# Performance work log

Measured on AMD Instinct MI355X. Metric: run time of the kernel, lower is better.

The kernel has to match this reference:

```python
import jax, jax.numpy as jnp
import numpy as np

N_HEADS, D_MODEL, D_HEAD = 16, 1024, 64
EPSILON = -100000.0  # module uses -1e5, not -inf
INIT_STD = 0.02


def setup_inputs() -> dict:
    key = jax.random.key(0)
    ks = jax.random.split(key, 5)
    B, S = 4, 2048
    x = jax.random.normal(ks[0], (B, S, D_MODEL), dtype=jnp.float32)
    W_Q = INIT_STD * jax.random.normal(ks[1], (N_HEADS, D_MODEL, D_HEAD), dtype=jnp.float32)
    W_K = INIT_STD * jax.random.normal(ks[2], (N_HEADS, D_MODEL, D_HEAD), dtype=jnp.float32)
    W_V = INIT_STD * jax.random.normal(ks[3], (N_HEADS, D_MODEL, D_HEAD), dtype=jnp.float32)
    W_O = INIT_STD * jax.random.normal(ks[4], (N_HEADS, D_HEAD, D_MODEL), dtype=jnp.float32)
    b_Q = jnp.zeros((N_HEADS, D_HEAD), jnp.float32)
    b_K = jnp.zeros((N_HEADS, D_HEAD), jnp.float32)
    b_V = jnp.zeros((N_HEADS, D_HEAD), jnp.float32)
    b_O = jnp.zeros((D_MODEL,), jnp.float32)
    return {"normalized_resid_pre": x, "W_Q": W_Q, "b_Q": b_Q, "W_K": W_K,
            "b_K": b_K, "W_V": W_V, "b_V": b_V, "W_O": W_O, "b_O": b_O}


def reference(normalized_resid_pre, W_Q, b_Q, W_K, b_K, W_V, b_V, W_O, b_O):
    x = normalized_resid_pre  # [b, s, e]
    q = jnp.einsum('bse,neh->bsnh', x, W_Q) + b_Q
    k = jnp.einsum('bse,neh->bsnh', x, W_K) + b_K
    v = jnp.einsum('bse,neh->bsnh', x, W_V) + b_V
    scores = jnp.einsum('bqnh,bknh->bnqk', q, k) / jnp.sqrt(jnp.float32(D_HEAD))
    sq, sk = scores.shape[-2], scores.shape[-1]
    causal = jnp.triu(jnp.ones((sq, sk), bool), k=1)  # True above diagonal
    scores = jnp.where(causal, jnp.float32(EPSILON), scores)
    probs = jax.nn.softmax(scores, axis=-1)
    z = jnp.einsum('bnqk,bknh->bqnh', probs, v)
    # sum over heads of per-head output projection + bias
    attn_out = jnp.einsum('bqnh,nhe->bqe', z, W_O) + b_O
    return attn_out
```

## Files before the change

kernel.cpp:

```cpp
#include <hip/hip_runtime.h>


typedef __attribute__((ext_vector_type(8))) short short8;
typedef __attribute__((ext_vector_type(4))) float floatx4;

#define SCL 0.1803368801111244f

__device__ __forceinline__ unsigned short f2bf(float f) {
  unsigned int x = __float_as_uint(f);
  x += 0x7fffu + ((x >> 16) & 1u);
  return (unsigned short)(x >> 16);
}

__device__ __forceinline__ void gload_lds16(const unsigned short* g, unsigned short* lds) {
  __builtin_amdgcn_global_load_lds(
      (const __attribute__((address_space(1))) void*)g,
      (__attribute__((address_space(3))) void*)lds, 16, 0, 0);
}

__global__ __launch_bounds__(256) void cvt_x_kernel(const float* __restrict__ X,
                                                    unsigned short* __restrict__ Xb) {
  int idx = ((blockIdx.x << 8) + threadIdx.x) << 2;
  float4 f = *(const float4*)(X + idx);
  unsigned short u[4] = { f2bf(f.x), f2bf(f.y), f2bf(f.z), f2bf(f.w) };
  *(uint2*)(Xb + idx) = *(uint2*)u;
}

__global__ __launch_bounds__(256) void transpose_wqkv3(
    const float* __restrict__ Wq, const float* __restrict__ Wk,
    const float* __restrict__ Wv, unsigned short* __restrict__ Bt) {
  __shared__ unsigned short T[64 * 72];
  const int t = threadIdx.x;
  const int e0 = blockIdx.x << 6, nn = blockIdx.y, proj = blockIdx.z;
  const float* W = (proj == 0) ? Wq : (proj == 1) ? Wk : Wv;
  const float* src = W + ((size_t)nn << 16) + ((size_t)e0 << 6);
#pragma unroll
  for (int rnd = 0; rnd < 4; ++rnd) {
    int off = (rnd << 10) + (t << 2);
    float4 f = *(const float4*)(src + off);
    int r = off >> 6, h = off & 63;
    T[r * 72 + h]     = f2bf(f.x);
    T[r * 72 + h + 1] = f2bf(f.y);
    T[r * 72 + h + 2] = f2bf(f.z);
    T[r * 72 + h + 3] = f2bf(f.w);
  }
  __syncthreads();
  const int h = t >> 2, ck = t & 3;
  size_t orow = ((size_t)((proj << 10) + (nn << 6) + h) << 10) + e0 + (ck << 4);
#pragma unroll
  for (int g = 0; g < 2; ++g) {
    unsigned short v[8];
#pragma unroll
    for (int j = 0; j < 8; ++j) v[j] = T[((ck << 4) + (g << 3) + j) * 72 + h];
    *(int4*)(Bt + orow + (g << 3)) = *(int4*)v;
  }
}

__global__ __launch_bounds__(256) void transpose_wo(const float* __restrict__ W,
                                                    unsigned short* __restrict__ Wt) {
  __shared__ unsigned short T[64 * 72];
  const int t = threadIdx.x;
  const int e0 = blockIdx.x << 6, k0 = blockIdx.y << 6;
#pragma unroll
  for (int rnd = 0; rnd < 4; ++rnd) {
    int r = (rnd << 4) + (t >> 4);
    int c = (t & 15) << 2;
    float4 f = *(const float4*)(W + ((size_t)(k0 + r) << 10) + e0 + c);
    T[r * 72 + c]     = f2bf(f.x);
    T[r * 72 + c + 1] = f2bf(f.y);
    T[r * 72 + c + 2] = f2bf(f.z);
    T[r * 72 + c + 3] = f2bf(f.w);
  }
  __syncthreads();
  const int i = t >> 2, ck = t & 3;
  size_t orow = ((size_t)(e0 + i) << 10) + k0 + (ck << 4);
#pragma unroll
  for (int g = 0; g < 2; ++g) {
    unsigned short v[8];
#pragma unroll
    for (int j = 0; j < 8; ++j) v[j] = T[((ck << 4) + (g << 3) + j) * 72 + i];
    *(int4*)(Wt + orow + (g << 3)) = *(int4*)v;
  }
}

template <int MODE>
__global__ __launch_bounds__(256) void gemm128_kernel(
    const unsigned short* __restrict__ A,
    const unsigned short* __restrict__ Bt,
    const float* __restrict__ b0, const float* __restrict__ b1,
    const float* __restrict__ b2,
    unsigned short* __restrict__ Oq, unsigned short* __restrict__ Ok,
    unsigned short* __restrict__ Ov, float* __restrict__ Of)
{
  const int K = 1024;
  __shared__ __align__(16) unsigned short As[4096];
  __shared__ __align__(16) unsigned short Bs[4096];
  const int tid = threadIdx.x;
  const int l   = tid & 63, w = tid >> 6;
  const int l15 = l & 15,  lg = l >> 4;
  const int mo  = (w >> 1) << 6, no = (w & 1) << 6;
  const int m0  = blockIdx.y << 7, n0 = blockIdx.x << 7;
  const int lrow = l >> 2;
  const int lcol = (l & 3) << 3;

  floatx4 acc[4][4];
#pragma unroll
  for (int i = 0; i < 4; ++i)
#pragma unroll
    for (int j = 0; j < 4; ++j) acc[i][j] = (floatx4){0.f, 0.f, 0.f, 0.f};

  for (int k0 = 0; k0 < K; k0 += 32) {
    __syncthreads();
#pragma unroll
    for (int j = 0; j < 2; ++j) {
      int seg = (w << 1) + j;
      int row = (seg << 4) + lrow;
      gload_lds16(A  + (size_t)(m0 + row) * K + k0 + lcol, &As[seg << 9]);
      gload_lds16(Bt + (size_t)(n0 + row) * K + k0 + lcol, &Bs[seg << 9]);
    }
    __syncthreads();
    short8 af[4], bf[4];
#pragma unroll
    for (int mc = 0; mc < 4; ++mc)
      af[mc] = *(const short8*)&As[((mo + (mc << 4) + l15) << 5) + (lg << 3)];
#pragma unroll
    for (int nc = 0; nc < 4; ++nc)
      bf[nc] = *(const short8*)&Bs[((no + (nc << 4) + l15) << 5) + (lg << 3)];
#pragma unroll
    for (int mc = 0; mc < 4; ++mc)
#pragma unroll
      for (int nc = 0; nc < 4; ++nc)
        acc[mc][nc] = __builtin_amdgcn_mfma_f32_16x16x32_bf16(af[mc], bf[nc], acc[mc][nc], 0, 0, 0);
  }

#pragma unroll
  for (int nc = 0; nc < 4; ++nc) {
    int c = n0 + no + (nc << 4) + l15;
    if (MODE == 1) {
      float bv = b0[c];
#pragma unroll
      for (int mc = 0; mc < 4; ++mc)
#pragma unroll
        for (int r = 0; r < 4; ++r) {
          int m = m0 + mo + (mc << 4) + (lg << 2) + r;
          Of[((size_t)m << 10) + c] = acc[mc][nc][r] + bv;
        }
    } else {
      int proj = c >> 10, cc = c & 1023;
      int hn = cc >> 6, h = cc & 63;
      const float* bp = (proj == 0) ? b0 : (proj == 1) ? b1 : b2;
      float bv = bp[cc];
      float sc = (proj == 0) ? SCL : 1.0f;
      if (proj < 2) {
        unsigned short* O = (proj == 0) ? Oq : Ok;
#pragma unroll
        for (int mc = 0; mc < 4; ++mc)
#pragma unroll
          for (int r = 0; r < 4; ++r) {
            int m = m0 + mo + (mc << 4) + (lg << 2) + r;
            int bb = m >> 11, ss = m & 2047;
            O[((((size_t)(bb << 4) + hn) << 11) + ss) * 64 + h] = f2bf((acc[mc][nc][r] + bv) * sc);
          }
      } else {
#pragma unroll
        for (int mc = 0; mc < 4; ++mc) {
          int m = m0 + mo + (mc << 4) + (lg << 2);
          int bb = m >> 11, ss = m & 2047;
          unsigned short p0 = f2bf(acc[mc][nc][0] + bv);
          unsigned short p1 = f2bf(acc[mc][nc][1] + bv);
          unsigned short p2 = f2bf(acc[mc][nc][2] + bv);
          unsigned short p3 = f2bf(acc[mc][nc][3] + bv);
          uint2 pk;
          pk.x = (unsigned int)p0 | ((unsigned int)p1 << 16);
          pk.y = (unsigned int)p2 | ((unsigned int)p3 << 16);
          *(uint2*)&Ov[((((size_t)(bb << 4) + hn) << 6) + h) * 2048 + ss] = pk;
        }
      }
    }
  }
}

__global__ __launch_bounds__(256, 2) void flash3_kernel(
    const unsigned short* __restrict__ Q,
    const unsigned short* __restrict__ K,
    const unsigned short* __restrict__ Vt,
    unsigned short* __restrict__ Z)
{
  __shared__ __align__(16) unsigned short Ks[4096];
  __shared__ __align__(16) unsigned short Vs[4096];
  __shared__ __align__(16) unsigned short Ps[4 * 2304];

  const int tid = threadIdx.x;
  const int l   = tid & 63, w = tid >> 6;
  const int l15 = l & 15,  lg = l >> 4;
  const int x    = blockIdx.x;
  const int head = ((x & 7) << 3) + ((x >> 6) & 7);
  const int pairidx = (x >> 3) & 7;
  const int n = head & 15, b = head >> 4;
  const size_t hoff = (size_t)head << 17;
  const unsigned short* Qh = Q + hoff;
  const unsigned short* Kh = K + hoff;
  const unsigned short* Vh = Vt + hoff;
  unsigned short* Psw = Ps + w * 2304;

  const int srow8 = l >> 3;
  const int sblk8 = ((l & 7) ^ srow8) << 3;
  const int swz   = l15 & 7;
  const int bo0   = (lg ^ swz) << 3;
  const int bo1   = ((4 + lg) ^ swz) << 3;

  short8 onef;
#pragma unroll
  for (int i = 0; i < 8; ++i) onef[i] = (short)0x3F80;

  for (int half = 0; half < 2; ++half) {
    const int qt  = half ? (15 - pairidx) : pairidx;
    const int q0w = (qt << 7) + (w << 5);

    short8 qf[2][2];
#pragma unroll
    for (int qc = 0; qc < 2; ++qc)
#pragma unroll
      for (int dh = 0; dh < 2; ++dh)
        qf[qc][dh] = *(const short8*)(Qh + (size_t)(q0w + (qc << 4) + l15) * 64 + (dh << 5) + (lg << 3));

    floatx4 acc_o[2][4], acc_l[2];
#pragma unroll
    for (int qc = 0; qc < 2; ++qc) {
      acc_l[qc] = (floatx4){0.f, 0.f, 0.f, 0.f};
#pragma unroll
      for (int dc = 0; dc < 4; ++dc) acc_o[qc][dc] = (floatx4){0.f, 0.f, 0.f, 0.f};
    }

    const int nkt = (qt << 1) + 2;
    for (int kt = 0; kt < nkt; ++kt) {
      const int k0 = kt << 6;
      __syncthreads();
#pragma unroll
      for (int j = 0; j < 2; ++j) {
        const int s = (w << 1) + j;
        gload_lds16(Kh + (size_t)(k0 + (s << 3) + srow8) * 64 + sblk8, &Ks[s << 9]);
        gload_lds16(Vh + (size_t)((s << 3) + srow8) * 2048 + k0 + sblk8, &Vs[s << 9]);
      }
      __syncthreads();
      if (k0 > q0w + 31) continue;

      floatx4 s0[4], s1[4];
#pragma unroll
      for (int mc = 0; mc < 4; ++mc) {
        s0[mc] = (floatx4){0.f, 0.f, 0.f, 0.f};
        s1[mc] = (floatx4){0.f, 0.f, 0.f, 0.f};
      }
#pragma unroll
      for (int dh = 0; dh < 2; ++dh) {
        const int bo = dh ? bo1 : bo0;
#pragma unroll
        for (int mc = 0; mc < 4; ++mc) {
          short8 ak = *(const short8*)&Ks[(((mc << 4) + l15) << 6) + bo];
          s0[mc] = __builtin_amdgcn_mfma_f32_16x16x32_bf16(ak, qf[0][dh], s0[mc], 0, 0, 0);
          s1[mc] = __builtin_amdgcn_mfma_f32_16x16x32_bf16(ak, qf[1][dh], s1[mc], 0, 0, 0);
        }
      }

      const bool needmask = (k0 + 63 > q0w);
#pragma unroll
      for (int qc = 0; qc < 2; ++qc) {
        const int qg = q0w + (qc << 4) + l15;
#pragma unroll
        for (int mc = 0; mc < 4; ++mc) {
          float p[4];
#pragma unroll
          for (int r = 0; r < 4; ++r) {
            float e = exp2f(qc ? s1[mc][r] : s0[mc][r]);
            if (needmask) {
              int key = k0 + (mc << 4) + (lg << 2) + r;
              e = (key > qg) ? 0.f : e;
            }
            p[r] = e;
          }
          uint2 pk;
          pk.x = (__float_as_uint(p[1]) & 0xFFFF0000u) | (__float_as_uint(p[0]) >> 16);
          pk.y = (__float_as_uint(p[3]) & 0xFFFF0000u) | (__float_as_uint(p[2]) >> 16);
          *(uint2*)&Psw[((qc << 4) + l15) * 72 + (mc << 4) + (lg << 2)] = pk;
        }
      }

      short8 pa[2][2];
#pragma unroll
      for (int qc = 0; qc < 2; ++qc)
#pragma unroll
        for (int kc = 0; kc < 2; ++kc)
          pa[qc][kc] = *(const short8*)&Psw[((qc << 4) + l15) * 72 + (kc << 5) + (lg << 3)];
#pragma unroll
      for (int kc = 0; kc < 2; ++kc) {
        const int bo = kc ? bo1 : bo0;
#pragma unroll
        for (int dc = 0; dc < 4; ++dc) {
          short8 vb = *(const short8*)&Vs[(((dc << 4) + l15) << 6) + bo];
          acc_o[0][dc] = __builtin_amdgcn_mfma_f32_16x16x32_bf16(pa[0][kc], vb, acc_o[0][dc], 0, 0, 0);
          acc_o[1][dc] = __builtin_amdgcn_mfma_f32_16x16x32_bf16(pa[1][kc], vb, acc_o[1][dc], 0, 0, 0);
        }
        acc_l[0] = __builtin_amdgcn_mfma_f32_16x16x32_bf16(pa[0][kc], onef, acc_l[0], 0, 0, 0);
        acc_l[1] = __builtin_amdgcn_mfma_f32_16x16x32_bf16(pa[1][kc], onef, acc_l[1], 0, 0, 0);
      }
    }

#pragma unroll
    for (int qc = 0; qc < 2; ++qc) {
      floatx4 inv;
#pragma unroll
      for (int r = 0; r < 4; ++r) inv[r] = 1.f / acc_l[qc][r];
#pragma unroll
      for (int dc = 0; dc < 4; ++dc)
#pragma unroll
        for (int r = 0; r < 4; ++r) {
          int qg = q0w + (qc << 4) + (lg << 2) + r;
          Z[(((size_t)b << 11) + qg) * 1024 + (n << 6) + (dc << 4) + l15] =
              f2bf(acc_o[qc][dc][r] * inv[r]);
        }
    }
  }
}

extern "C" void kernel_launch(void* const* d_in, const int* in_sizes, int n_in,
                              void* d_out, int out_size, void* d_ws, size_t ws_size,
                              hipStream_t stream) {
  const float* x   = (const float*)d_in[0];
  const float* W_Q = (const float*)d_in[1];
  const float* b_Q = (const float*)d_in[2];
  const float* W_K = (const float*)d_in[3];
  const float* b_K = (const float*)d_in[4];
  const float* W_V = (const float*)d_in[5];
  const float* b_V = (const float*)d_in[6];
  const float* W_O = (const float*)d_in[7];
  const float* b_O = (const float*)d_in[8];
  float* out = (float*)d_out;

  unsigned short* ws    = (unsigned short*)d_ws;
  unsigned short* BtQKV = ws;
  unsigned short* Wo_t  = BtQKV + (3u << 20);
  unsigned short* Xb    = Wo_t + (1u << 20);
  unsigned short* Qb    = Xb + (8u << 20);
  unsigned short* Kb    = Qb + (8u << 20);
  unsigned short* Vtb   = Kb + (8u << 20);
  unsigned short* Zb    = Vtb + (8u << 20);

  cvt_x_kernel   <<<8192, 256, 0, stream>>>(x, Xb);
  transpose_wqkv3<<<dim3(16, 16, 3), 256, 0, stream>>>(W_Q, W_K, W_V, BtQKV);
  transpose_wo   <<<dim3(16, 16), 256, 0, stream>>>(W_O, Wo_t);

  gemm128_kernel<0><<<dim3(24, 64), 256, 0, stream>>>(
      Xb, BtQKV, b_Q, b_K, b_V, Qb, Kb, Vtb, nullptr);

  flash3_kernel<<<512, 256, 0, stream>>>(Qb, Kb, Vtb, Zb);

  gemm128_kernel<1><<<dim3(8, 64), 256, 0, stream>>>(
      Zb, Wo_t, b_O, nullptr, nullptr, nullptr, nullptr, nullptr, out);
}
```

Measured before the change: 285.3 us.

## Fuse prep kernels, deepen GEMM K-tile with swizzle, split flash into per-tile blocks

The three prep kernels (x conversion, QKV weight transpose, W_O transpose) become a single launch that branches on block index, saving launch overhead. The GEMM now loads a 64-wide K tile per iteration into XOR-swizzled LDS, halving barriers and cutting bank conflicts at the cost of twice the LDS. The flash kernel no longer pairs two query tiles per block; it launches 1024 blocks, one query tile each, heaviest tiles first, and drops the occupancy hint, giving better parallelism but possibly less balanced tail work.

Result: slower. 299.2 us (+4.9%).

```diff
diff --git a/kernel.cpp b/kernel.cpp
--- a/kernel.cpp
+++ b/kernel.cpp
@@ -18,68 +18,67 @@
       (__attribute__((address_space(3))) void*)lds, 16, 0, 0);
 }
 
-__global__ __launch_bounds__(256) void cvt_x_kernel(const float* __restrict__ X,
-                                                    unsigned short* __restrict__ Xb) {
-  int idx = ((blockIdx.x << 8) + threadIdx.x) << 2;
-  float4 f = *(const float4*)(X + idx);
-  unsigned short u[4] = { f2bf(f.x), f2bf(f.y), f2bf(f.z), f2bf(f.w) };
-  *(uint2*)(Xb + idx) = *(uint2*)u;
-}
-
-__global__ __launch_bounds__(256) void transpose_wqkv3(
+__global__ __launch_bounds__(256) void prep_kernel(
+    const float* __restrict__ X,  unsigned short* __restrict__ Xb,
     const float* __restrict__ Wq, const float* __restrict__ Wk,
-    const float* __restrict__ Wv, unsigned short* __restrict__ Bt) {
+    const float* __restrict__ Wv, unsigned short* __restrict__ Bt,
+    const float* __restrict__ Wo, unsigned short* __restrict__ Wt)
+{
   __shared__ unsigned short T[64 * 72];
-  const int t = threadIdx.x;
-  const int e0 = blockIdx.x << 6, nn = blockIdx.y, proj = blockIdx.z;
-  const float* W = (proj == 0) ? Wq : (proj == 1) ? Wk : Wv;
-  const float* src = W + ((size_t)nn << 16) + ((size_t)e0 << 6);
-#pragma unroll
-  for (int rnd = 0; rnd < 4; ++rnd) {
-    int off = (rnd << 10) + (t << 2);
-    float4 f = *(const float4*)(src + off);
-    int r = off >> 6, h = off & 63;
-    T[r * 72 + h]     = f2bf(f.x);
-    T[r * 72 + h + 1] = f2bf(f.y);
-    T[r * 72 + h + 2] = f2bf(f.z);
-    T[r * 72 + h + 3] = f2bf(f.w);
-  }
-  __syncthreads();
-  const int h = t >> 2, ck = t & 3;
-  size_t orow = ((size_t)((proj << 10) + (nn << 6) + h) << 10) + e0 + (ck << 4);
-#pragma unroll
-  for (int g = 0; g < 2; ++g) {
-    unsigned short v[8];
-#pragma unroll
-    for (int j = 0; j < 8; ++j) v[j] = T[((ck << 4) + (g << 3) + j) * 72 + h];
-    *(int4*)(Bt + orow + (g << 3)) = *(int4*)v;
-  }
-}
-
-__global__ __launch_bounds__(256) void transpose_wo(const float* __restrict__ W,
-                                                    unsigned short* __restrict__ Wt) {
-  __shared__ unsigned short T[64 * 72];
-  const int t = threadIdx.x;
-  const int e0 = blockIdx.x << 6, k0 = blockIdx.y << 6;
-#pragma unroll
-  for (int rnd = 0; rnd < 4; ++rnd) {
-    int r = (rnd << 4) + (t >> 4);
-    int c = (t & 15) << 2;
-    float4 f = *(const float4*)(W + ((size_t)(k0 + r) << 10) + e0 + c);
-    T[r * 72 + c]     = f2bf(f.x);
-    T[r * 72 + c + 1] = f2bf(f.y);
-    T[r * 72 + c + 2] = f2bf(f.z);
-    T[r * 72 + c + 3] = f2bf(f.w);
-  }
-  __syncthreads();
-  const int i = t >> 2, ck = t & 3;
-  size_t orow = ((size_t)(e0 + i) << 10) + k0 + (ck << 4);
-#pragma unroll
-  for (int g = 0; g < 2; ++g) {
-    unsigned short v[8];
-#pragma unroll
-    for (int j = 0; j < 8; ++j) v[j] = T[((ck << 4) + (g << 3) + j) * 72 + i];
-    *(int4*)(Wt + orow + (g << 3)) = *(int4*)v;
+  const int bid = blockIdx.x, t = threadIdx.x;
+  if (bid < 8192) {
+    int idx = ((bid << 8) + t) << 2;
+    float4 f = *(const float4*)(X + idx);
+    unsigned short u[4] = { f2bf(f.x), f2bf(f.y), f2bf(f.z), f2bf(f.w) };
+    *(uint2*)(Xb + idx) = *(uint2*)u;
+  } else if (bid < 8960) {
+    int b2 = bid - 8192;
+    int e0 = (b2 & 15) << 6, nn = (b2 >> 4) & 15, proj = b2 >> 8;
+    const float* W = (proj == 0) ? Wq : (proj == 1) ? Wk : Wv;
+    const float* src = W + ((size_t)nn << 16) + ((size_t)e0 << 6);
+#pragma unroll
+    for (int rnd = 0; rnd < 4; ++rnd) {
+      int off = (rnd << 10) + (t << 2);
+      float4 f = *(const float4*)(src + off);
+      int r = off >> 6, h = off & 63;
+      T[r * 72 + h]     = f2bf(f.x);
+      T[r * 72 + h + 1] = f2bf(f.y);
+      T[r * 72 + h + 2] = f2bf(f.z);
+      T[r * 72 + h + 3] = f2bf(f.w);
+    }
+    __syncthreads();
+    const int h = t >> 2, ck = t & 3;
+    size_t orow = ((size_t)((proj << 10) + (nn << 6) + h) << 10) + e0 + (ck << 4);
+#pragma unroll
+    for (int g = 0; g < 2; ++g) {
+      unsigned short v[8];
+#pragma unroll
+      for (int j = 0; j < 8; ++j) v[j] = T[((ck << 4) + (g << 3) + j) * 72 + h];
+      *(int4*)(Bt + orow + (g << 3)) = *(int4*)v;
+    }
+  } else {
+    int b2 = bid - 8960;
+    int e0 = (b2 & 15) << 6, k0 = (b2 >> 4) << 6;
+#pragma unroll
+    for (int rnd = 0; rnd < 4; ++rnd) {
+      int r = (rnd << 4) + (t >> 4);
+      int c = (t & 15) << 2;
+      float4 f = *(const float4*)(Wo + ((size_t)(k0 + r) << 10) + e0 + c);
+      T[r * 72 + c]     = f2bf(f.x);
+      T[r * 72 + c + 1] = f2bf(f.y);
+      T[r * 72 + c + 2] = f2bf(f.z);
+      T[r * 72 + c + 3] = f2bf(f.w);
+    }
+    __syncthreads();
+    const int i = t >> 2, ck = t & 3;
+    size_t orow = ((size_t)(e0 + i) << 10) + k0 + (ck << 4);
+#pragma unroll
+    for (int g = 0; g < 2; ++g) {
+      unsigned short v[8];
+#pragma unroll
+      for (int j = 0; j < 8; ++j) v[j] = T[((ck << 4) + (g << 3) + j) * 72 + i];
+      *(int4*)(Wt + orow + (g << 3)) = *(int4*)v;
+    }
   }
 }
 
@@ -93,15 +92,16 @@
     unsigned short* __restrict__ Ov, float* __restrict__ Of)
 {
   const int K = 1024;
-  __shared__ __align__(16) unsigned short As[4096];
-  __shared__ __align__(16) unsigned short Bs[4096];
+  __shared__ __align__(16) unsigned short As[8192];
+  __shared__ __align__(16) unsigned short Bs[8192];
   const int tid = threadIdx.x;
   const int l   = tid & 63, w = tid >> 6;
   const int l15 = l & 15,  lg = l >> 4;
   const int mo  = (w >> 1) << 6, no = (w & 1) << 6;
   const int m0  = blockIdx.y << 7, n0 = blockIdx.x << 7;
-  const int lrow = l >> 2;
-  const int lcol = (l & 3) << 3;
+  const int srow = l >> 3;
+  const int gblk = ((l & 7) ^ srow) << 3;
+  const int rsw  = l15 & 7;
 
   floatx4 acc[4][4];
 #pragma unroll
@@ -109,28 +109,31 @@
 #pragma unroll
     for (int j = 0; j < 4; ++j) acc[i][j] = (floatx4){0.f, 0.f, 0.f, 0.f};
 
-  for (int k0 = 0; k0 < K; k0 += 32) {
-    __syncthreads();
-#pragma unroll
-    for (int j = 0; j < 2; ++j) {
-      int seg = (w << 1) + j;
-      int row = (seg << 4) + lrow;
-      gload_lds16(A  + (size_t)(m0 + row) * K + k0 + lcol, &As[seg << 9]);
-      gload_lds16(Bt + (size_t)(n0 + row) * K + k0 + lcol, &Bs[seg << 9]);
-    }
-    __syncthreads();
-    short8 af[4], bf[4];
-#pragma unroll
-    for (int mc = 0; mc < 4; ++mc)
-      af[mc] = *(const short8*)&As[((mo + (mc << 4) + l15) << 5) + (lg << 3)];
-#pragma unroll
-    for (int nc = 0; nc < 4; ++nc)
-      bf[nc] = *(const short8*)&Bs[((no + (nc << 4) + l15) << 5) + (lg << 3)];
-#pragma unroll
-    for (int mc = 0; mc < 4; ++mc)
+  for (int k0 = 0; k0 < K; k0 += 64) {
+    __syncthreads();
+#pragma unroll
+    for (int s = 0; s < 4; ++s) {
+      const int br = (s << 5) + (w << 3);
+      gload_lds16(A  + (size_t)(m0 + br + srow) * K + k0 + gblk, &As[br << 6]);
+      gload_lds16(Bt + (size_t)(n0 + br + srow) * K + k0 + gblk, &Bs[br << 6]);
+    }
+    __syncthreads();
+#pragma unroll
+    for (int kh = 0; kh < 2; ++kh) {
+      const int bo = (((kh << 2) + lg) ^ rsw) << 3;
+      short8 af[4], bf[4];
+#pragma unroll
+      for (int mc = 0; mc < 4; ++mc)
+        af[mc] = *(const short8*)&As[((mo + (mc << 4) + l15) << 6) + bo];
 #pragma unroll
       for (int nc = 0; nc < 4; ++nc)
-        acc[mc][nc] = __builtin_amdgcn_mfma_f32_16x16x32_bf16(af[mc], bf[nc], acc[mc][nc], 0, 0, 0);
+        bf[nc] = *(const short8*)&Bs[((no + (nc << 4) + l15) << 6) + bo];
+#pragma unroll
+      for (int mc = 0; mc < 4; ++mc)
+#pragma unroll
+        for (int nc = 0; nc < 4; ++nc)
+          acc[mc][nc] = __builtin_amdgcn_mfma_f32_16x16x32_bf16(af[mc], bf[nc], acc[mc][nc], 0, 0, 0);
+    }
   }
 
 #pragma unroll
@@ -180,7 +183,7 @@
   }
 }
 
-__global__ __launch_bounds__(256, 2) void flash3_kernel(
+__global__ __launch_bounds__(256) void flash4_kernel(
     const unsigned short* __restrict__ Q,
     const unsigned short* __restrict__ K,
     const unsigned short* __restrict__ Vt,
@@ -194,8 +197,8 @@
   const int l   = tid & 63, w = tid >> 6;
   const int l15 = l & 15,  lg = l >> 4;
   const int x    = blockIdx.x;
-  const int head = ((x & 7) << 3) + ((x >> 6) & 7);
-  const int pairidx = (x >> 3) & 7;
+  const int qt   = 15 - ((x >> 3) & 15);
+  const int head = ((x & 7) << 3) + (x >> 7);
   const int n = head & 15, b = head >> 4;
   const size_t hoff = (size_t)head << 17;
   const unsigned short* Qh = Q + hoff;
@@ -213,112 +216,109 @@
 #pragma unroll
   for (int i = 0; i < 8; ++i) onef[i] = (short)0x3F80;
 
-  for (int half = 0; half < 2; ++half) {
-    const int qt  = half ? (15 - pairidx) : pairidx;
-    const int q0w = (qt << 7) + (w << 5);
-
-    short8 qf[2][2];
+  const int q0w = (qt << 7) + (w << 5);
+
+  short8 qf[2][2];
+#pragma unroll
+  for (int qc = 0; qc < 2; ++qc)
+#pragma unroll
+    for (int dh = 0; dh < 2; ++dh)
+      qf[qc][dh] = *(const short8*)(Qh + (size_t)(q0w + (qc << 4) + l15) * 64 + (dh << 5) + (lg << 3));
+
+  floatx4 acc_o[2][4], acc_l[2];
+#pragma unroll
+  for (int qc = 0; qc < 2; ++qc) {
+    acc_l[qc] = (floatx4){0.f, 0.f, 0.f, 0.f};
+#pragma unroll
+    for (int dc = 0; dc < 4; ++dc) acc_o[qc][dc] = (floatx4){0.f, 0.f, 0.f, 0.f};
+  }
+
+  const int nkt = (qt << 1) + 2;
+  for (int kt = 0; kt < nkt; ++kt) {
+    const int k0 = kt << 6;
+    __syncthreads();
+#pragma unroll
+    for (int j = 0; j < 2; ++j) {
+      const int s = (w << 1) + j;
+      gload_lds16(Kh + (size_t)(k0 + (s << 3) + srow8) * 64 + sblk8, &Ks[s << 9]);
+      gload_lds16(Vh + (size_t)((s << 3) + srow8) * 2048 + k0 + sblk8, &Vs[s << 9]);
+    }
+    __syncthreads();
+    if (k0 > q0w + 31) continue;
+
+    floatx4 s0[4], s1[4];
+#pragma unroll
+    for (int mc = 0; mc < 4; ++mc) {
+      s0[mc] = (floatx4){0.f, 0.f, 0.f, 0.f};
+      s1[mc] = (floatx4){0.f, 0.f, 0.f, 0.f};
+    }
+#pragma unroll
+    for (int dh = 0; dh < 2; ++dh) {
+      const int bo = dh ? bo1 : bo0;
+#pragma unroll
+      for (int mc = 0; mc < 4; ++mc) {
+        short8 ak = *(const short8*)&Ks[(((mc << 4) + l15) << 6) + bo];
+        s0[mc] = __builtin_amdgcn_mfma_f32_16x16x32_bf16(ak, qf[0][dh], s0[mc], 0, 0, 0);
+        s1[mc] = __builtin_amdgcn_mfma_f32_16x16x32_bf16(ak, qf[1][dh], s1[mc], 0, 0, 0);
+      }
+    }
+
+    const bool needmask = (k0 + 63 > q0w);
+#pragma unroll
+    for (int qc = 0; qc < 2; ++qc) {
+      const int qg = q0w + (qc << 4) + l15;
+#pragma unroll
+      for (int mc = 0; mc < 4; ++mc) {
+        float p[4];
+#pragma unroll
+        for (int r = 0; r < 4; ++r) {
+          float e = exp2f(qc ? s1[mc][r] : s0[mc][r]);
+          if (needmask) {
+            int key = k0 + (mc << 4) + (lg << 2) + r;
+            e = (key > qg) ? 0.f : e;
+          }
+          p[r] = e;
+        }
+        uint2 pk;
+        pk.x = (__float_as_uint(p[1]) & 0xFFFF0000u) | (__float_as_uint(p[0]) >> 16);
+        pk.y = (__float_as_uint(p[3]) & 0xFFFF0000u) | (__float_as_uint(p[2]) >> 16);
+        *(uint2*)&Psw[((qc << 4) + l15) * 72 + (mc << 4) + (lg << 2)] = pk;
+      }
+    }
+
+    short8 pa[2][2];
 #pragma unroll
     for (int qc = 0; qc < 2; ++qc)
 #pragma unroll
-      for (int dh = 0; dh < 2; ++dh)
-        qf[qc][dh] = *(const short8*)(Qh + (size_t)(q0w + (qc << 4) + l15) * 64 + (dh << 5) + (lg << 3));
-
-    floatx4 acc_o[2][4], acc_l[2];
-#pragma unroll
-    for (int qc = 0; qc < 2; ++qc) {
-      acc_l[qc] = (floatx4){0.f, 0.f, 0.f, 0.f};
-#pragma unroll
-      for (int dc = 0; dc < 4; ++dc) acc_o[qc][dc] = (floatx4){0.f, 0.f, 0.f, 0.f};
-    }
-
-    const int nkt = (qt << 1) + 2;
-    for (int kt = 0; kt < nkt; ++kt) {
-      const int k0 = kt << 6;
-      __syncthreads();
-#pragma unroll
-      for (int j = 0; j < 2; ++j) {
-        const int s = (w << 1) + j;
-        gload_lds16(Kh + (size_t)(k0 + (s << 3) + srow8) * 64 + sblk8, &Ks[s << 9]);
-        gload_lds16(Vh + (size_t)((s << 3) + srow8) * 2048 + k0 + sblk8, &Vs[s << 9]);
-      }
-      __syncthreads();
-      if (k0 > q0w + 31) continue;
-
-      floatx4 s0[4], s1[4];
-#pragma unroll
-      for (int mc = 0; mc < 4; ++mc) {
-        s0[mc] = (floatx4){0.f, 0.f, 0.f, 0.f};
-        s1[mc] = (floatx4){0.f, 0.f, 0.f, 0.f};
-      }
-#pragma unroll
-      for (int dh = 0; dh < 2; ++dh) {
-        const int bo = dh ? bo1 : bo0;
-#pragma unroll
-        for (int mc = 0; mc < 4; ++mc) {
-          short8 ak = *(const short8*)&Ks[(((mc << 4) + l15) << 6) + bo];
-          s0[mc] = __builtin_amdgcn_mfma_f32_16x16x32_bf16(ak, qf[0][dh], s0[mc], 0, 0, 0);
-          s1[mc] = __builtin_amdgcn_mfma_f32_16x16x32_bf16(ak, qf[1][dh], s1[mc], 0, 0, 0);
-        }
-      }
-
-      const bool needmask = (k0 + 63 > q0w);
-#pragma unroll
-      for (int qc = 0; qc < 2; ++qc) {
-        const int qg = q0w + (qc << 4) + l15;
-#pragma unroll
-        for (int mc = 0; mc < 4; ++mc) {
-          float p[4];
-#pragma unroll
-          for (int r = 0; r < 4; ++r) {
-            float e = exp2f(qc ? s1[mc][r] : s0[mc][r]);
-            if (needmask) {
-              int key = k0 + (mc << 4) + (lg << 2) + r;
-              e = (key > qg) ? 0.f : e;
-            }
-            p[r] = e;
-          }
-          uint2 pk;
-          pk.x = (__float_as_uint(p[1]) & 0xFFFF0000u) | (__float_as_uint(p[0]) >> 16);
-          pk.y = (__float_as_uint(p[3]) & 0xFFFF0000u) | (__float_as_uint(p[2]) >> 16);
-          *(uint2*)&Psw[((qc << 4) + l15) * 72 + (mc << 4) + (lg << 2)] = pk;
-        }
-      }
-
-      short8 pa[2][2];
-#pragma unroll
-      for (int qc = 0; qc < 2; ++qc)
-#pragma unroll
-        for (int kc = 0; kc < 2; ++kc)
-          pa[qc][kc] = *(const short8*)&Psw[((qc << 4) + l15) * 72 + (kc << 5) + (lg << 3)];
-#pragma unroll
-      for (int kc = 0; kc < 2; ++kc) {
-        const int bo = kc ? bo1 : bo0;
-#pragma unroll
-        for (int dc = 0; dc < 4; ++dc) {
-          short8 vb = *(const short8*)&Vs[(((dc << 4) + l15) << 6) + bo];
-          acc_o[0][dc] = __builtin_amdgcn_mfma_f32_16x16x32_bf16(pa[0][kc], vb, acc_o[0][dc], 0, 0, 0);
-          acc_o[1][dc] = __builtin_amdgcn_mfma_f32_16x16x32_bf16(pa[1][kc], vb, acc_o[1][dc], 0, 0, 0);
-        }
-        acc_l[0] = __builtin_amdgcn_mfma_f32_16x16x32_bf16(pa[0][kc], onef, acc_l[0], 0, 0, 0);
-        acc_l[1] = __builtin_amdgcn_mfma_f32_16x16x32_bf16(pa[1][kc], onef, acc_l[1], 0, 0, 0);
-      }
-    }
-
-#pragma unroll
-    for (int qc = 0; qc < 2; ++qc) {
-      floatx4 inv;
-#pragma unroll
-      for (int r = 0; r < 4; ++r) inv[r] = 1.f / acc_l[qc][r];
-#pragma unroll
-      for (int dc = 0; dc < 4; ++dc)
-#pragma unroll
-        for (int r = 0; r < 4; ++r) {
-          int qg = q0w + (qc << 4) + (lg << 2) + r;
-          Z[(((size_t)b << 11) + qg) * 1024 + (n << 6) + (dc << 4) + l15] =
-              f2bf(acc_o[qc][dc][r] * inv[r]);
-        }
-    }
+      for (int kc = 0; kc < 2; ++kc)
+        pa[qc][kc] = *(const short8*)&Psw[((qc << 4) + l15) * 72 + (kc << 5) + (lg << 3)];
+#pragma unroll
+    for (int kc = 0; kc < 2; ++kc) {
+      const int bo = kc ? bo1 : bo0;
+#pragma unroll
+      for (int dc = 0; dc < 4; ++dc) {
+        short8 vb = *(const short8*)&Vs[(((dc << 4) + l15) << 6) + bo];
+        acc_o[0][dc] = __builtin_amdgcn_mfma_f32_16x16x32_bf16(pa[0][kc], vb, acc_o[0][dc], 0, 0, 0);
+        acc_o[1][dc] = __builtin_amdgcn_mfma_f32_16x16x32_bf16(pa[1][kc], vb, acc_o[1][dc], 0, 0, 0);
+      }
+      acc_l[0] = __builtin_amdgcn_mfma_f32_16x16x32_bf16(pa[0][kc], onef, acc_l[0], 0, 0, 0);
+      acc_l[1] = __builtin_amdgcn_mfma_f32_16x16x32_bf16(pa[1][kc], onef, acc_l[1], 0, 0, 0);
+    }
+  }
+
+#pragma unroll
+  for (int qc = 0; qc < 2; ++qc) {
+    floatx4 inv;
+#pragma unroll
+    for (int r = 0; r < 4; ++r) inv[r] = 1.f / acc_l[qc][r];
+#pragma unroll
+    for (int dc = 0; dc < 4; ++dc)
+#pragma unroll
+      for (int r = 0; r < 4; ++r) {
+        int qg = q0w + (qc << 4) + (lg << 2) + r;
+        Z[(((size_t)b << 11) + qg) * 1024 + (n << 6) + (dc << 4) + l15] =
+            f2bf(acc_o[qc][dc][r] * inv[r]);
+      }
   }
 }
 
@@ -345,14 +345,12 @@
   unsigned short* Vtb   = Kb + (8u << 20);
   unsigned short* Zb    = Vtb + (8u << 20);
 
-  cvt_x_kernel   <<<8192, 256, 0, stream>>>(x, Xb);
-  transpose_wqkv3<<<dim3(16, 16, 3), 256, 0, stream>>>(W_Q, W_K, W_V, BtQKV);
-  transpose_wo   <<<dim3(16, 16), 256, 0, stream>>>(W_O, Wo_t);
+  prep_kernel<<<9216, 256, 0, stream>>>(x, Xb, W_Q, W_K, W_V, BtQKV, W_O, Wo_t);
 
   gemm128_kernel<0><<<dim3(24, 64), 256, 0, stream>>>(
       Xb, BtQKV, b_Q, b_K, b_V, Qb, Kb, Vtb, nullptr);
 
-  flash3_kernel<<<512, 256, 0, stream>>>(Qb, Kb, Vtb, Zb);
+  flash4_kernel<<<1024, 256, 0, stream>>>(Qb, Kb, Vtb, Zb);
 
   gemm128_kernel<1><<<dim3(8, 64), 256, 0, stream>>>(
       Zb, Wo_t, b_O, nullptr, nullptr, nullptr, nullptr, nullptr, out);
```
